# Optimization experiments

Hardware: AMD Instinct MI355X
Metric: run time of the kernel (lower is better)

## Reference

```python
import jax, jax.numpy as jnp
import numpy as np

L, H, NH, NKV, HD, I, MAXS = 5, 1024, 16, 8, 128, 3072, 16
EPS = 1e-6
THETA = 1000000.0
N_REP = NH // NKV


def rms(x, w, eps=EPS):
    # RMSNorm over last dim (fp32 math as in the torch module)
    return w * (x * jax.lax.rsqrt(jnp.mean(x * x, axis=-1, keepdims=True) + eps))


def rotate_half(v):
    d = v.shape[-1] // 2
    return jnp.concatenate([-v[..., d:], v[..., :d]], axis=-1)


def setup_inputs() -> dict:
    key = jax.random.key(0)
    ks = jax.random.split(key, 20)
    s = 0.02
    inp = {
        'hidden_states': jax.random.normal(ks[0], (1, 1, H), jnp.float32),
        'position_id': jax.random.randint(ks[1], (1,), 0, MAXS, jnp.int64) if jax.config.jax_enable_x64 else jax.random.randint(ks[1], (1,), 0, MAXS).astype(jnp.int32),
        'past_keys': jax.random.normal(ks[2], (L, 1, NKV, MAXS, HD), jnp.float32),
        'past_values': jax.random.normal(ks[3], (L, 1, NKV, MAXS, HD), jnp.float32),
        'w_iln': jnp.ones((L, H), jnp.float32),
        'w_paln': jnp.ones((L, H), jnp.float32),
        'wq': jax.random.normal(ks[4], (L, NH * HD, H), jnp.float32) * s,
        'wk': jax.random.normal(ks[5], (L, NKV * HD, H), jnp.float32) * s,
        'wv': jax.random.normal(ks[6], (L, NKV * HD, H), jnp.float32) * s,
        'wo': jax.random.normal(ks[7], (L, H, NH * HD), jnp.float32) * s,
        'w_qn': jnp.ones((L, HD), jnp.float32),
        'w_kn': jnp.ones((L, HD), jnp.float32),
        'w_gate': jax.random.normal(ks[8], (L, I, H), jnp.float32) * s,
        'w_up': jax.random.normal(ks[9], (L, I, H), jnp.float32) * s,
        'w_down': jax.random.normal(ks[10], (L, H, I), jnp.float32) * s,
        'w_onorm': jnp.ones((H,), jnp.float32),
    }
    return inp


def reference(hidden_states, position_id, past_keys, past_values,
              w_iln, w_paln, wq, wk, wv, wo, w_qn, w_kn,
              w_gate, w_up, w_down, w_onorm):
    pos = position_id[0]
    # RoPE tables at the single decode position
    inv_freq = 1.0 / (THETA ** (jnp.arange(0, HD, 2, dtype=jnp.float32) / HD))  # [HD/2]
    freqs = pos.astype(jnp.float32) * inv_freq
    cos = jnp.concatenate([jnp.cos(freqs)] * 2)  # [HD]
    sin = jnp.concatenate([jnp.sin(freqs)] * 2)
    mask = jnp.arange(MAXS) > pos  # [MAXS] future positions masked
    scale = 1.0 / jnp.sqrt(jnp.float32(HD))

    x = hidden_states[0, 0]  # [H]

    def layer(x, xs):
        pk, pv, wi, wp, q_, k_, v_, o_, qn, kn, g_, u_, d_ = xs
        h = rms(x, wi)
        q = (q_ @ h).reshape(NH, HD)
        k_new = rms((k_ @ h).reshape(NKV, HD), kn)
        v_new = (v_ @ h).reshape(NKV, HD)
        q = rms(q, qn)
        q = q * cos + rotate_half(q) * sin
        k_new = k_new * cos + rotate_half(k_new) * sin
        # write new K/V at pos into the fixed-size cache
        kc = pk[0].at[:, pos, :].set(k_new)  # [NKV, MAXS, HD]
        vc = pv[0].at[:, pos, :].set(v_new)
        # GQA: repeat each kv head N_REP times (contiguous, matching torch expand)
        ke = jnp.repeat(kc, N_REP, axis=0)  # [NH, MAXS, HD]
        ve = jnp.repeat(vc, N_REP, axis=0)
        scores = jnp.einsum('hd,hkd->hk', q, ke) * scale
        scores = jnp.where(mask[None, :], -jnp.inf, scores)
        p = jax.nn.softmax(scores, axis=-1)
        attn = jnp.einsum('hk,hkd->hd', p, ve).reshape(NH * HD)
        x = x + o_ @ attn
        h = rms(x, wp)
        x = x + d_ @ (jax.nn.silu(g_ @ h) * (u_ @ h))
        return x, (kc[None], vc[None])

    xs = (past_keys, past_values, w_iln, w_paln, wq, wk, wv, wo,
          w_qn, w_kn, w_gate, w_up, w_down)
    x, (pks, pvs) = jax.lax.scan(layer, x, xs)
    out = rms(x, w_onorm)[None, None, :]  # [1,1,H]
    return out, pks, pvs


if __name__ == '__main__':
    o = reference(**setup_inputs())
    print(o[0].shape, o[1].shape, o[2].shape)
```

## Files before the change

kernel.cpp:

```cpp
#include <hip/hip_runtime.h>
#include <hip/hip_bf16.h>
#include <math.h>

typedef __hip_bfloat16 bf16;
typedef unsigned long long ull;

#define L_    5
#define H_    1024
#define NH_   16
#define NKV_  8
#define HD_   128
#define I_    3072
#define MAXS_ 16
#define EPS_  1e-6f
#define KVE_  (L_ * NKV_ * MAXS_ * HD_)
#define GRID_ 512
#define SS_OFF  10240
#define BAR_OFF 10496
#define PF_BYTES 49152

typedef __attribute__((address_space(1))) void as1_void;
typedef __attribute__((address_space(3))) void as3_void;

static __device__ __forceinline__ float bl(unsigned u){ return __uint_as_float(u << 16); }
static __device__ __forceinline__ float bh(unsigned u){ return __uint_as_float(u & 0xffff0000u); }

static __device__ __forceinline__ float wred(float v){
#pragma unroll
    for (int o = 32; o; o >>= 1) v += __shfl_xor(v, o, 64);
    return v;
}

static __device__ __forceinline__ float dot8(uint4 u, float4 a, float4 b){
    return bl(u.x)*a.x + bh(u.x)*a.y + bl(u.y)*a.z + bh(u.y)*a.w
         + bl(u.z)*b.x + bh(u.z)*b.y + bl(u.w)*b.z + bh(u.w)*b.w;
}

static __device__ __forceinline__ float rms_inv(float sumsq, float n){
    float a = sumsq / n + EPS_;
    float y = rsqrtf(a);
    y = y * (1.5f - 0.5f * a * y * y);
    return y;
}

static __device__ __forceinline__ float gld(const float* p){
    return __hip_atomic_load((float*)p, __ATOMIC_RELAXED, __HIP_MEMORY_SCOPE_AGENT);
}
static __device__ __forceinline__ void gst(float* p, float v){
    __hip_atomic_store(p, v, __ATOMIC_RELAXED, __HIP_MEMORY_SCOPE_AGENT);
}
static __device__ __forceinline__ void gst8(ull* p, ull v){
    __hip_atomic_store(p, v, __ATOMIC_RELAXED, __HIP_MEMORY_SCOPE_AGENT);
}

static __device__ __forceinline__ void waitc(unsigned* c, unsigned tgt){
    while (__hip_atomic_load(c, __ATOMIC_RELAXED, __HIP_MEMORY_SCOPE_AGENT) < tgt)
        __builtin_amdgcn_s_sleep(1);
}
static __device__ __forceinline__ void incc(unsigned* c){
    __hip_atomic_fetch_add(c, 1u, __ATOMIC_RELAXED, __HIP_MEMORY_SCOPE_AGENT);
}

static __device__ __forceinline__ float ld1(const void* p, size_t i, bool b16){
    return b16 ? __uint_as_float((unsigned)((const ushort*)p)[i] << 16) : ((const float*)p)[i];
}
static __device__ __forceinline__ void st1(void* p, size_t i, float v, bool b16){
    if (b16) ((bf16*)p)[i] = __float2bfloat16(v);
    else     ((float*)p)[i] = v;
}

template<bool B16>
static __device__ __forceinline__ void pf_stage(const void* w, size_t elemoff,
                                                char* ldst, int nelem, int lane){
    const int ESZ = B16 ? 2 : 4;
    const char* g = (const char*)w + elemoff * (size_t)ESZ + (size_t)lane * 16;
    const int bytes = nelem * ESZ;
#pragma unroll
    for (int c = 0; c < bytes; c += 1024)
        __builtin_amdgcn_global_load_lds((const as1_void*)(g + c),
                                         (as3_void*)(ldst + c), 16, 0, 0);
}

template<bool B16>
static __device__ __forceinline__ float pf_dot(const char* pfrow, const float* hs,
                                               int nelem, int lane){
    float acc = 0.f;
    if (B16) {
#pragma unroll
        for (int c = 0; c < nelem / 512; c++) {
            uint4 u = *(const uint4*)(pfrow + c * 1024 + lane * 16);
            const float4* h4 = (const float4*)&hs[c * 512 + lane * 8];
            acc += dot8(u, h4[0], h4[1]);
        }
    } else {
#pragma unroll
        for (int c = 0; c < nelem / 256; c++) {
            float4 f = *(const float4*)(pfrow + c * 1024 + lane * 16);
            const float4* h = (const float4*)&hs[c * 256 + lane * 4];
            acc += f.x*h->x + f.y*h->y + f.z*h->z + f.w*h->w;
        }
    }
    return acc;
}

static __device__ __forceinline__ void q_addr(int r, int l,
        const void* wq, const void* wk, const void* wv,
        float* qraw, float* kraw, float* vraw,
        const void*& w, size_t& off, float*& dst){
    if (r < NH_ * HD_) {
        w = wq; off = (size_t)l * NH_ * HD_ * H_ + (size_t)r * H_; dst = qraw + r;
    } else if (r < NH_ * HD_ + NKV_ * HD_) {
        int rk = r - NH_ * HD_;
        w = wk; off = (size_t)l * NKV_ * HD_ * H_ + (size_t)rk * H_; dst = kraw + rk;
    } else {
        int rv = r - NH_ * HD_ - NKV_ * HD_;
        w = wv; off = (size_t)l * NKV_ * HD_ * H_ + (size_t)rv * H_; dst = vraw + rv;
    }
}

__global__ void k_zero(float* __restrict__ ws){
    int t = threadIdx.x;
    if (t < 16) ws[SS_OFF + t] = 0.f;
    unsigned* bar = (unsigned*)(ws + BAR_OFF);
    for (int i = t; i < 192; i += 256) bar[i] = 0u;
}

template<bool B16>
static __device__ __forceinline__ void run(
        const void* hid, int pos,
        const void* pk, const void* pv,
        const void* w_iln, const void* w_paln,
        const void* wq, const void* wk, const void* wv, const void* wo,
        const void* w_qn, const void* w_kn,
        const void* w_gate, const void* w_up, const void* w_down,
        const void* w_onorm,
        float* ws, void* out,
        float* sh, float* red, float* s_inv_p, char* pf)
{
    const int ESZ = B16 ? 2 : 4;
    const int gid = blockIdx.x, tid = threadIdx.x;
    const int lane = tid & 63, wid = tid >> 6;

    float* x    = ws;
    float* qraw = ws + 1024;
    float* kraw = ws + 3072;
    float* vraw = ws + 4096;
    float* attn = ws + 5120;
    float* act  = ws + 7168;
    float* ss   = ws + SS_OFF;
    unsigned* bar  = (unsigned*)(ws + BAR_OFF);
    unsigned* icnt = bar;
    unsigned* qcnt = bar + 32;
    unsigned* acnt = bar + 64;
    unsigned* ocnt = bar + 96;
    unsigned* gcnt = bar + 128;
    unsigned* dcnt = bar + 160;

    auto PFQ = [&](int ll){
        const void* w; size_t off; float* dst;
        q_addr(gid * 8 + wid, ll, wq, wk, wv, qraw, kraw, vraw, w, off, dst);
        pf_stage<B16>(w, off, pf + (size_t)wid * 1024 * ESZ, 1024, lane);
        q_addr(gid * 8 + wid + 4, ll, wq, wk, wv, qraw, kraw, vraw, w, off, dst);
        pf_stage<B16>(w, off, pf + (size_t)(wid + 4) * 1024 * ESZ, 1024, lane);
    };
    auto PFO = [&](int ll){
        pf_stage<B16>(wo, (size_t)ll * H_ * NH_ * HD_ + (size_t)(gid * 4 + wid) * NH_ * HD_,
                      pf + (size_t)wid * 2048 * ESZ, 2048, lane);
    };
    auto PFG = [&](int ll){
        int i0 = gid * 6 + wid;
        size_t offg = (size_t)ll * I_ * H_ + (size_t)i0 * H_;
        pf_stage<B16>(w_gate, offg, pf + (size_t)(2 * wid)     * 1024 * ESZ, 1024, lane);
        pf_stage<B16>(w_up,   offg, pf + (size_t)(2 * wid + 1) * 1024 * ESZ, 1024, lane);
        if (wid < 2) {
            size_t offh = (size_t)ll * I_ * H_ + (size_t)(i0 + 4) * H_;
            pf_stage<B16>(w_gate, offh, pf + (size_t)(8 + 2 * wid) * 1024 * ESZ, 1024, lane);
            pf_stage<B16>(w_up,   offh, pf + (size_t)(9 + 2 * wid) * 1024 * ESZ, 1024, lane);
        }
    };
    auto PFD = [&](int ll){
        pf_stage<B16>(w_down, (size_t)ll * H_ * I_ + (size_t)(gid * 4 + wid) * I_,
                      pf + (size_t)wid * 3072 * ESZ, 3072, lane);
    };

    PFQ(0);
    {
        const size_t nll = (size_t)KVE_ * ESZ / 8;
        const ull* sk = (const ull*)pk;
        const ull* sv = (const ull*)pv;
        ull* dk = (ull*)((char*)out + (size_t)H_ * ESZ);
        ull* dv = dk + nll;
        for (size_t i = (size_t)gid * 256 + tid; i < nll; i += (size_t)GRID_ * 256) {
            gst8(dk + i, sk[i]);
            gst8(dv + i, sv[i]);
        }
        if (gid == 0) {
            float s0 = 0.f;
            for (int j = tid; j < H_; j += 256) {
                float v = ld1(hid, j, B16);
                gst(&x[j], v); s0 += v * v;
            }
            s0 = wred(s0);
            if (lane == 0) red[wid] = s0;
            __syncthreads();
            if (tid == 0) gst(&ss[0], red[0] + red[1] + red[2] + red[3]);
        }
        __syncthreads();
        if (tid == 0) {
            asm volatile("s_waitcnt vmcnt(0)" ::: "memory");
            incc(icnt);
        }
    }

    for (int l = 0; l < L_; ++l) {
        if (tid == 0) {
            if (l == 0) waitc(icnt, (unsigned)GRID_);
            else        waitc(dcnt, 256u * l);
            *s_inv_p = rms_inv(gld(&ss[2 * l]), (float)H_);
        }
        __syncthreads();
        {
            float inv = *s_inv_p;
            for (int j = tid; j < H_; j += 256)
                sh[j] = gld(&x[j]) * inv * ld1(w_iln, (size_t)l * H_ + j, B16);
        }
        __syncthreads();
        asm volatile("s_waitcnt vmcnt(0)" ::: "memory");
        {
            const void* w; size_t off; float* dst;
            q_addr(gid * 8 + wid, l, wq, wk, wv, qraw, kraw, vraw, w, off, dst);
            float acc = wred(pf_dot<B16>(pf + (size_t)wid * 1024 * ESZ, sh, 1024, lane));
            if (lane == 0) gst(dst, acc);
            q_addr(gid * 8 + wid + 4, l, wq, wk, wv, qraw, kraw, vraw, w, off, dst);
            acc = wred(pf_dot<B16>(pf + (size_t)(wid + 4) * 1024 * ESZ, sh, 1024, lane));
            if (lane == 0) gst(dst, acc);
        }
        __syncthreads();
        if (tid == 0) incc(qcnt);

        if (gid < 256) PFO(l); else PFG(l);

        if (gid < NH_ && wid == 0) {
            waitc(qcnt, 512u * (l + 1));
            int hh = gid, g = hh >> 1;
            float fr = (float)pos * exp2f(-(float)lane * 0.31143075889569023f);
            float c = cosf(fr), s = sinf(fr);

            float q0 = gld(&qraw[hh * HD_ + lane]), q1 = gld(&qraw[hh * HD_ + 64 + lane]);
            float qi = rms_inv(wred(q0 * q0 + q1 * q1), (float)HD_);
            q0 *= qi * ld1(w_qn, (size_t)l * HD_ + lane, B16);
            q1 *= qi * ld1(w_qn, (size_t)l * HD_ + 64 + lane, B16);
            float q0r = q0 * c - q1 * s, q1r = q1 * c + q0 * s;

            float k0 = gld(&kraw[g * HD_ + lane]), k1 = gld(&kraw[g * HD_ + 64 + lane]);
            float ki = rms_inv(wred(k0 * k0 + k1 * k1), (float)HD_);
            k0 *= ki * ld1(w_kn, (size_t)l * HD_ + lane, B16);
            k1 *= ki * ld1(w_kn, (size_t)l * HD_ + 64 + lane, B16);
            float k0r = k0 * c - k1 * s, k1r = k1 * c + k0 * s;

            float v0 = gld(&vraw[g * HD_ + lane]), v1 = gld(&vraw[g * HD_ + 64 + lane]);

            size_t kco = H_ + (size_t)l * NKV_ * MAXS_ * HD_ + (size_t)g * MAXS_ * HD_;
            size_t vco = kco + KVE_;
            const float scale = 0.08838834764831845f;

            float scb[MAXS_];
            float m = -3.0e38f;
#pragma unroll
            for (int t = 0; t < MAXS_; t++) {
                float d = (t == pos)
                    ? (q0r * k0r + q1r * k1r)
                    : (q0r * ld1(out, kco + t * HD_ + lane, B16)
                     + q1r * ld1(out, kco + t * HD_ + 64 + lane, B16));
                d = wred(d) * scale;
                scb[t] = d;
                if (t <= pos) m = fmaxf(m, d);
            }
            float se = 0.f;
#pragma unroll
            for (int t = 0; t < MAXS_; t++) {
                float e = (t <= pos) ? expf(scb[t] - m) : 0.0f;
                scb[t] = e; se += e;
            }
            float rinv = 1.0f / se;
            float a0 = 0.f, a1 = 0.f;
#pragma unroll
            for (int t = 0; t < MAXS_; t++) {
                float pt = scb[t] * rinv;
                if (t == pos) { a0 += pt * v0; a1 += pt * v1; }
                else {
                    a0 += pt * ld1(out, vco + t * HD_ + lane, B16);
                    a1 += pt * ld1(out, vco + t * HD_ + 64 + lane, B16);
                }
            }
            gst(&attn[hh * HD_ + lane],      a0);
            gst(&attn[hh * HD_ + 64 + lane], a1);
            if ((hh & 1) == 0) {
                st1(out, kco + pos * HD_ + lane,      k0r, B16);
                st1(out, kco + pos * HD_ + 64 + lane, k1r, B16);
                st1(out, vco + pos * HD_ + lane,      v0,  B16);
                st1(out, vco + pos * HD_ + 64 + lane, v1,  B16);
            }
            asm volatile("s_waitcnt vmcnt(0)" ::: "memory");
            if (lane == 0) incc(acnt);
        }

        if (gid < 256) {
            if (tid == 0) waitc(acnt, 16u * (l + 1));
            __syncthreads();
            for (int j = tid; j < NH_ * HD_; j += 256) sh[j] = gld(&attn[j]);
            __syncthreads();
            asm volatile("s_waitcnt vmcnt(0)" ::: "memory");
            int r = gid * 4 + wid;
            float acc = wred(pf_dot<B16>(pf + (size_t)wid * 2048 * ESZ, sh, 2048, lane));
            if (lane == 0) {
                float xn = gld(&x[r]) + acc;
                gst(&x[r], xn);
                red[wid] = xn * xn;
            }
            __syncthreads();
            if (tid == 0) {
                atomicAdd(&ss[2 * l + 1], red[0] + red[1] + red[2] + red[3]);
                asm volatile("s_waitcnt vmcnt(0)" ::: "memory");
                incc(ocnt);
            }
            __syncthreads();
            PFG(l);
        }

        if (tid == 0) {
            waitc(ocnt, 256u * (l + 1));
            *s_inv_p = rms_inv(gld(&ss[2 * l + 1]), (float)H_);
        }
        __syncthreads();
        {
            float inv = *s_inv_p;
            for (int j = tid; j < H_; j += 256)
                sh[j] = gld(&x[j]) * inv * ld1(w_paln, (size_t)l * H_ + j, B16);
        }
        __syncthreads();
        asm volatile("s_waitcnt vmcnt(0)" ::: "memory");
        {
            int i0 = gid * 6 + wid;
            float ag = wred(pf_dot<B16>(pf + (size_t)(2 * wid)     * 1024 * ESZ, sh, 1024, lane));
            float au = wred(pf_dot<B16>(pf + (size_t)(2 * wid + 1) * 1024 * ESZ, sh, 1024, lane));
            if (lane == 0) {
                float sig = 1.0f / (1.0f + expf(-ag));
                gst(&act[i0], ag * sig * au);
            }
            if (wid < 2) {
                ag = wred(pf_dot<B16>(pf + (size_t)(8 + 2 * wid) * 1024 * ESZ, sh, 1024, lane));
                au = wred(pf_dot<B16>(pf + (size_t)(9 + 2 * wid) * 1024 * ESZ, sh, 1024, lane));
                if (lane == 0) {
                    float sig = 1.0f / (1.0f + expf(-ag));
                    gst(&act[i0 + 4], ag * sig * au);
                }
            }
        }
        __syncthreads();
        if (tid == 0) incc(gcnt);

        if (gid < 256) PFD(l);
        else if (l + 1 < L_) PFQ(l + 1);

        if (gid < 256) {
            if (tid == 0) waitc(gcnt, 512u * (l + 1));
            __syncthreads();
            for (int j = tid; j < I_; j += 256) sh[j] = gld(&act[j]);
            __syncthreads();
            asm volatile("s_waitcnt vmcnt(0)" ::: "memory");
            int r = gid * 4 + wid;
            float acc = wred(pf_dot<B16>(pf + (size_t)wid * 3072 * ESZ, sh, 3072, lane));
            if (lane == 0) {
                float xn = gld(&x[r]) + acc;
                gst(&x[r], xn);
                red[wid] = xn * xn;
            }
            __syncthreads();
            if (tid == 0) {
                atomicAdd(&ss[2 * l + 2], red[0] + red[1] + red[2] + red[3]);
                asm volatile("s_waitcnt vmcnt(0)" ::: "memory");
                incc(dcnt);
            }
            __syncthreads();
            if (l + 1 < L_) PFQ(l + 1);
        }
    }

    if (gid == 0) {
        if (tid == 0) {
            waitc(dcnt, 256u * L_);
            *s_inv_p = rms_inv(gld(&ss[2 * L_]), (float)H_);
        }
        __syncthreads();
        float inv = *s_inv_p;
        for (int j = tid; j < H_; j += 256)
            st1(out, j, gld(&x[j]) * inv * ld1(w_onorm, j, B16), B16);
    }
}

__global__ __launch_bounds__(256, 2) void k_model(
        const void* __restrict__ hid, const int* __restrict__ pos_p,
        const void* __restrict__ pk,  const void* __restrict__ pv,
        const void* __restrict__ w_iln, const void* __restrict__ w_paln,
        const void* __restrict__ wq,  const void* __restrict__ wk,
        const void* __restrict__ wv,  const void* __restrict__ wo,
        const void* __restrict__ w_qn, const void* __restrict__ w_kn,
        const void* __restrict__ w_gate, const void* __restrict__ w_up,
        const void* __restrict__ w_down, const void* __restrict__ w_onorm,
        float* __restrict__ ws, void* __restrict__ out)
{
    __shared__ float sh[I_];
    __shared__ float red[4];
    __shared__ float s_inv;
    __shared__ __align__(16) char pf[PF_BYTES];

    const bool b16 = (((const ushort*)w_onorm)[0] == 0x3F80);
    int pos = pos_p[0];
    pos = pos < 0 ? 0 : (pos > MAXS_ - 1 ? MAXS_ - 1 : pos);

    if (b16)
        run<true>(hid, pos, pk, pv, w_iln, w_paln, wq, wk, wv, wo,
                  w_qn, w_kn, w_gate, w_up, w_down, w_onorm,
                  ws, out, sh, red, &s_inv, pf);
    else
        run<false>(hid, pos, pk, pv, w_iln, w_paln, wq, wk, wv, wo,
                   w_qn, w_kn, w_gate, w_up, w_down, w_onorm,
                   ws, out, sh, red, &s_inv, pf);
}

extern "C" void kernel_launch(void* const* d_in, const int* in_sizes, int n_in,
                              void* d_out, int out_size, void* d_ws, size_t ws_size,
                              hipStream_t stream) {
    const void* hid     = d_in[0];
    const int*  pos     = (const int*)d_in[1];
    const void* pk      = d_in[2];
    const void* pv      = d_in[3];
    const void* w_iln   = d_in[4];
    const void* w_paln  = d_in[5];
    const void* wq      = d_in[6];
    const void* wk      = d_in[7];
    const void* wv      = d_in[8];
    const void* wo      = d_in[9];
    const void* w_qn    = d_in[10];
    const void* w_kn    = d_in[11];
    const void* w_gate  = d_in[12];
    const void* w_up    = d_in[13];
    const void* w_down  = d_in[14];
    const void* w_onorm = d_in[15];
    float* ws = (float*)d_ws;

    k_zero<<<1, 256, 0, stream>>>(ws);
    k_model<<<GRID_, 256, 0, stream>>>(hid, pos, pk, pv, w_iln, w_paln,
                                       wq, wk, wv, wo, w_qn, w_kn,
                                       w_gate, w_up, w_down, w_onorm,
                                       ws, d_out);
}
```

Before: 526.2 us.

## Decouple KV cache copy from grid barrier and vectorize shared-buffer loads with acquire fences

Result: slower. 718.2 us (+36.5%).

```diff
diff --git a/kernel.cpp b/kernel.cpp
--- a/kernel.cpp
+++ b/kernel.cpp
@@ -49,13 +49,20 @@
 static __device__ __forceinline__ void gst(float* p, float v){
     __hip_atomic_store(p, v, __ATOMIC_RELAXED, __HIP_MEMORY_SCOPE_AGENT);
 }
+static __device__ __forceinline__ void gstu(unsigned* p, unsigned v){
+    __hip_atomic_store(p, v, __ATOMIC_RELAXED, __HIP_MEMORY_SCOPE_AGENT);
+}
 static __device__ __forceinline__ void gst8(ull* p, ull v){
     __hip_atomic_store(p, v, __ATOMIC_RELAXED, __HIP_MEMORY_SCOPE_AGENT);
 }
 
+static __device__ __forceinline__ void acq(){
+    __builtin_amdgcn_fence(__ATOMIC_ACQUIRE, "agent");
+}
+
 static __device__ __forceinline__ void waitc(unsigned* c, unsigned tgt){
     while (__hip_atomic_load(c, __ATOMIC_RELAXED, __HIP_MEMORY_SCOPE_AGENT) < tgt)
-        __builtin_amdgcn_s_sleep(1);
+        __builtin_amdgcn_s_sleep(2);
 }
 static __device__ __forceinline__ void incc(unsigned* c){
     __hip_atomic_fetch_add(c, 1u, __ATOMIC_RELAXED, __HIP_MEMORY_SCOPE_AGENT);
@@ -67,6 +74,18 @@
 static __device__ __forceinline__ void st1(void* p, size_t i, float v, bool b16){
     if (b16) ((bf16*)p)[i] = __float2bfloat16(v);
     else     ((float*)p)[i] = v;
+}
+
+static __device__ __forceinline__ float4 ld4(const void* p, size_t i4, bool b16){
+    if (b16) {
+        uint2 u = ((const uint2*)p)[i4];
+        return make_float4(bl(u.x), bh(u.x), bl(u.y), bh(u.y));
+    }
+    return ((const float4*)p)[i4];
+}
+
+static __device__ __forceinline__ unsigned bfbits(float v){
+    return (unsigned)__builtin_bit_cast(unsigned short, __float2bfloat16(v));
 }
 
 template<bool B16>
@@ -184,29 +203,33 @@
     };
 
     PFQ(0);
+
     {
+        const int shift = B16 ? 5 : 6;
         const size_t nll = (size_t)KVE_ * ESZ / 8;
         const ull* sk = (const ull*)pk;
         const ull* sv = (const ull*)pv;
         ull* dk = (ull*)((char*)out + (size_t)H_ * ESZ);
         ull* dv = dk + nll;
         for (size_t i = (size_t)gid * 256 + tid; i < nll; i += (size_t)GRID_ * 256) {
-            gst8(dk + i, sk[i]);
-            gst8(dv + i, sv[i]);
-        }
-        if (gid == 0) {
-            float s0 = 0.f;
-            for (int j = tid; j < H_; j += 256) {
-                float v = ld1(hid, j, B16);
-                gst(&x[j], v); s0 += v * v;
-            }
-            s0 = wred(s0);
-            if (lane == 0) red[wid] = s0;
-            __syncthreads();
-            if (tid == 0) gst(&ss[0], red[0] + red[1] + red[2] + red[3]);
-        }
+            if ((int)((i >> shift) & (MAXS_ - 1)) != pos) {
+                gst8(dk + i, sk[i]);
+                gst8(dv + i, sv[i]);
+            }
+        }
+    }
+
+    if (gid == 0) {
+        float s0 = 0.f;
+        for (int j = tid; j < H_; j += 256) {
+            float v = ld1(hid, j, B16);
+            gst(&x[j], v); s0 += v * v;
+        }
+        s0 = wred(s0);
+        if (lane == 0) red[wid] = s0;
         __syncthreads();
         if (tid == 0) {
+            gst(&ss[0], red[0] + red[1] + red[2] + red[3]);
             asm volatile("s_waitcnt vmcnt(0)" ::: "memory");
             incc(icnt);
         }
@@ -214,15 +237,18 @@
 
     for (int l = 0; l < L_; ++l) {
         if (tid == 0) {
-            if (l == 0) waitc(icnt, (unsigned)GRID_);
+            if (l == 0) waitc(icnt, 1u);
             else        waitc(dcnt, 256u * l);
             *s_inv_p = rms_inv(gld(&ss[2 * l]), (float)H_);
         }
         __syncthreads();
+        acq();
         {
             float inv = *s_inv_p;
-            for (int j = tid; j < H_; j += 256)
-                sh[j] = gld(&x[j]) * inv * ld1(w_iln, (size_t)l * H_ + j, B16);
+            float4 xv = ((const float4*)x)[tid];
+            float4 wv = ld4(w_iln, (size_t)l * (H_ / 4) + tid, B16);
+            ((float4*)sh)[tid] = make_float4(xv.x * inv * wv.x, xv.y * inv * wv.y,
+                                             xv.z * inv * wv.z, xv.w * inv * wv.w);
         }
         __syncthreads();
         asm volatile("s_waitcnt vmcnt(0)" ::: "memory");
@@ -241,27 +267,27 @@
         if (gid < 256) PFO(l); else PFG(l);
 
         if (gid < NH_ && wid == 0) {
-            waitc(qcnt, 512u * (l + 1));
+            if (lane == 0) waitc(qcnt, 512u * (l + 1));
+            acq();
             int hh = gid, g = hh >> 1;
             float fr = (float)pos * exp2f(-(float)lane * 0.31143075889569023f);
             float c = cosf(fr), s = sinf(fr);
 
-            float q0 = gld(&qraw[hh * HD_ + lane]), q1 = gld(&qraw[hh * HD_ + 64 + lane]);
+            float q0 = qraw[hh * HD_ + lane], q1 = qraw[hh * HD_ + 64 + lane];
             float qi = rms_inv(wred(q0 * q0 + q1 * q1), (float)HD_);
             q0 *= qi * ld1(w_qn, (size_t)l * HD_ + lane, B16);
             q1 *= qi * ld1(w_qn, (size_t)l * HD_ + 64 + lane, B16);
             float q0r = q0 * c - q1 * s, q1r = q1 * c + q0 * s;
 
-            float k0 = gld(&kraw[g * HD_ + lane]), k1 = gld(&kraw[g * HD_ + 64 + lane]);
+            float k0 = kraw[g * HD_ + lane], k1 = kraw[g * HD_ + 64 + lane];
             float ki = rms_inv(wred(k0 * k0 + k1 * k1), (float)HD_);
             k0 *= ki * ld1(w_kn, (size_t)l * HD_ + lane, B16);
             k1 *= ki * ld1(w_kn, (size_t)l * HD_ + 64 + lane, B16);
             float k0r = k0 * c - k1 * s, k1r = k1 * c + k0 * s;
 
-            float v0 = gld(&vraw[g * HD_ + lane]), v1 = gld(&vraw[g * HD_ + 64 + lane]);
-
-            size_t kco = H_ + (size_t)l * NKV_ * MAXS_ * HD_ + (size_t)g * MAXS_ * HD_;
-            size_t vco = kco + KVE_;
+            float v0 = vraw[g * HD_ + lane], v1 = vraw[g * HD_ + 64 + lane];
+
+            size_t slc = ((size_t)l * NKV_ + g) * MAXS_ * HD_;
             const float scale = 0.08838834764831845f;
 
             float scb[MAXS_];
@@ -270,8 +296,8 @@
             for (int t = 0; t < MAXS_; t++) {
                 float d = (t == pos)
                     ? (q0r * k0r + q1r * k1r)
-                    : (q0r * ld1(out, kco + t * HD_ + lane, B16)
-                     + q1r * ld1(out, kco + t * HD_ + 64 + lane, B16));
+                    : (q0r * ld1(pk, slc + t * HD_ + lane, B16)
+                     + q1r * ld1(pk, slc + t * HD_ + 64 + lane, B16));
                 d = wred(d) * scale;
                 scb[t] = d;
                 if (t <= pos) m = fmaxf(m, d);
@@ -289,17 +315,39 @@
                 float pt = scb[t] * rinv;
                 if (t == pos) { a0 += pt * v0; a1 += pt * v1; }
                 else {
-                    a0 += pt * ld1(out, vco + t * HD_ + lane, B16);
-                    a1 += pt * ld1(out, vco + t * HD_ + 64 + lane, B16);
+                    a0 += pt * ld1(pv, slc + t * HD_ + lane, B16);
+                    a1 += pt * ld1(pv, slc + t * HD_ + 64 + lane, B16);
                 }
             }
             gst(&attn[hh * HD_ + lane],      a0);
             gst(&attn[hh * HD_ + 64 + lane], a1);
+
             if ((hh & 1) == 0) {
-                st1(out, kco + pos * HD_ + lane,      k0r, B16);
-                st1(out, kco + pos * HD_ + 64 + lane, k1r, B16);
-                st1(out, vco + pos * HD_ + lane,      v0,  B16);
-                st1(out, vco + pos * HD_ + 64 + lane, v1,  B16);
+                size_t kco = H_ + slc, vco = kco + (size_t)KVE_;
+                if (B16) {
+                    unsigned kb0 = bfbits(k0r), kb1 = bfbits(k1r);
+                    unsigned vb0 = bfbits(v0),  vb1 = bfbits(v1);
+                    int s0i = (lane & 31) * 2, s1i = s0i + 1;
+                    unsigned ka = (unsigned)__shfl((int)kb0, s0i, 64);
+                    unsigned kb = (unsigned)__shfl((int)kb0, s1i, 64);
+                    unsigned kc = (unsigned)__shfl((int)kb1, s0i, 64);
+                    unsigned kd = (unsigned)__shfl((int)kb1, s1i, 64);
+                    unsigned va = (unsigned)__shfl((int)vb0, s0i, 64);
+                    unsigned vb = (unsigned)__shfl((int)vb0, s1i, 64);
+                    unsigned vc = (unsigned)__shfl((int)vb1, s0i, 64);
+                    unsigned vd = (unsigned)__shfl((int)vb1, s1i, 64);
+                    unsigned kw = (lane < 32) ? (ka | (kb << 16)) : (kc | (kd << 16));
+                    unsigned vw = (lane < 32) ? (va | (vb << 16)) : (vc | (vd << 16));
+                    unsigned* ob = (unsigned*)out;
+                    gstu(ob + (kco + pos * HD_) / 2 + lane, kw);
+                    gstu(ob + (vco + pos * HD_) / 2 + lane, vw);
+                } else {
+                    float* ob = (float*)out;
+                    gst(ob + kco + pos * HD_ + lane,      k0r);
+                    gst(ob + kco + pos * HD_ + 64 + lane, k1r);
+                    gst(ob + vco + pos * HD_ + lane,      v0);
+                    gst(ob + vco + pos * HD_ + 64 + lane, v1);
+                }
             }
             asm volatile("s_waitcnt vmcnt(0)" ::: "memory");
             if (lane == 0) incc(acnt);
@@ -308,13 +356,15 @@
         if (gid < 256) {
             if (tid == 0) waitc(acnt, 16u * (l + 1));
             __syncthreads();
-            for (int j = tid; j < NH_ * HD_; j += 256) sh[j] = gld(&attn[j]);
+            acq();
+            ((float4*)sh)[tid]       = ((const float4*)attn)[tid];
+            ((float4*)sh)[tid + 256] = ((const float4*)attn)[tid + 256];
             __syncthreads();
             asm volatile("s_waitcnt vmcnt(0)" ::: "memory");
             int r = gid * 4 + wid;
             float acc = wred(pf_dot<B16>(pf + (size_t)wid * 2048 * ESZ, sh, 2048, lane));
             if (lane == 0) {
-                float xn = gld(&x[r]) + acc;
+                float xn = ((const float*)x)[r] + acc;
                 gst(&x[r], xn);
                 red[wid] = xn * xn;
             }
@@ -333,10 +383,13 @@
             *s_inv_p = rms_inv(gld(&ss[2 * l + 1]), (float)H_);
         }
         __syncthreads();
+        acq();
         {
             float inv = *s_inv_p;
-            for (int j = tid; j < H_; j += 256)
-                sh[j] = gld(&x[j]) * inv * ld1(w_paln, (size_t)l * H_ + j, B16);
+            float4 xv = ((const float4*)x)[tid];
+            float4 wv = ld4(w_paln, (size_t)l * (H_ / 4) + tid, B16);
+            ((float4*)sh)[tid] = make_float4(xv.x * inv * wv.x, xv.y * inv * wv.y,
+                                             xv.z * inv * wv.z, xv.w * inv * wv.w);
         }
         __syncthreads();
         asm volatile("s_waitcnt vmcnt(0)" ::: "memory");
@@ -366,13 +419,16 @@
         if (gid < 256) {
             if (tid == 0) waitc(gcnt, 512u * (l + 1));
             __syncthreads();
-            for (int j = tid; j < I_; j += 256) sh[j] = gld(&act[j]);
+            acq();
+            ((float4*)sh)[tid]       = ((const float4*)act)[tid];
+            ((float4*)sh)[tid + 256] = ((const float4*)act)[tid + 256];
+            ((float4*)sh)[tid + 512] = ((const float4*)act)[tid + 512];
             __syncthreads();
             asm volatile("s_waitcnt vmcnt(0)" ::: "memory");
             int r = gid * 4 + wid;
             float acc = wred(pf_dot<B16>(pf + (size_t)wid * 3072 * ESZ, sh, 3072, lane));
             if (lane == 0) {
-                float xn = gld(&x[r]) + acc;
+                float xn = ((const float*)x)[r] + acc;
                 gst(&x[r], xn);
                 red[wid] = xn * xn;
             }
@@ -393,9 +449,10 @@
             *s_inv_p = rms_inv(gld(&ss[2 * L_]), (float)H_);
         }
         __syncthreads();
+        acq();
         float inv = *s_inv_p;
         for (int j = tid; j < H_; j += 256)
-            st1(out, j, gld(&x[j]) * inv * ld1(w_onorm, j, B16), B16);
+            st1(out, j, ((const float*)x)[j] * inv * ld1(w_onorm, j, B16), B16);
     }
 }
 
```
